# Performance work log

Measured on AMD Instinct MI355X. Metric: run time of the kernel, lower is better.

The kernel has to match this reference:

```python
import jax, jax.numpy as jnp
import numpy as np

N, E, D, H = 50000, 1600000, 256, 256
EPS = 1e-5

def prelu(x, a):
    return jnp.where(x >= 0, x, a * x)

def batch_norm(x, gamma, beta):
    # training-mode BatchNorm1d: stats over the node (batch) dim
    mu = jnp.mean(x, axis=0)
    var = jnp.var(x, axis=0)
    return (x - mu) * jax.lax.rsqrt(var + EPS) * gamma + beta

def gcn_conv(x, edge_index, W, b):
    # PyG GCNConv: h = XW, add self-loops, symmetric norm, scatter-add, + bias
    h = x @ W
    n = x.shape[0]
    row = jnp.concatenate([edge_index[0], jnp.arange(n)])
    col = jnp.concatenate([edge_index[1], jnp.arange(n)])
    w = jnp.ones(row.shape[0], dtype=x.dtype)
    deg = jax.ops.segment_sum(w, col, num_segments=n)
    dinv = jnp.where(deg > 0, jax.lax.rsqrt(deg), 0.0)
    norm = dinv[row] * w * dinv[col]  # [E+N]
    msg = h[row] * norm[:, None]      # [E+N, H] gathered messages
    out = jax.ops.segment_sum(msg, col, num_segments=n)
    return out + b

def setup_inputs() -> dict:
    key = jax.random.key(0)
    ks = jax.random.split(key, 10)
    x = jax.random.normal(ks[0], (N, D), dtype=jnp.float32)
    edge_index = jax.random.randint(ks[1], (2, E), 0, N).astype(jnp.int64)
    s1 = 1.0 / np.sqrt(D)
    s2 = 1.0 / np.sqrt(H)
    return {
        "x": x,
        "edge_index": edge_index,
        "W1": jax.random.uniform(ks[2], (D, H), jnp.float32, -s1, s1),
        "b1": jnp.zeros((H,), jnp.float32),
        "W2": jax.random.uniform(ks[3], (H, H), jnp.float32, -s2, s2),
        "b2": jnp.zeros((H,), jnp.float32),
        "prelu_a": jnp.asarray(0.25, jnp.float32),
        "bn_gamma": jnp.ones((H,), jnp.float32),
        "bn_beta": jnp.zeros((H,), jnp.float32),
        "proj_W": jax.random.uniform(ks[4], (H, H), jnp.float32, -s2, s2),
        "proj_b": jnp.zeros((H,), jnp.float32),
        "pbn_gamma": jnp.ones((H,), jnp.float32),
        "pbn_beta": jnp.zeros((H,), jnp.float32),
        "prelu2_a": jnp.asarray(0.25, jnp.float32),
    }

def reference(x, edge_index, W1, b1, W2, b2, prelu_a, bn_gamma, bn_beta,
              proj_W, proj_b, pbn_gamma, pbn_beta, prelu2_a):
    # eval-mode dropout (identity); BN uses batch stats
    z = prelu(gcn_conv(x, edge_index, W1, b1), prelu_a)
    z = prelu(gcn_conv(z, edge_index, W2, b2), prelu_a)
    z = batch_norm(z, bn_gamma, bn_beta)
    p = prelu(batch_norm(z @ proj_W + proj_b, pbn_gamma, pbn_beta), prelu2_a)
    return (z, p)
```

## Files before the change

### kernel.cpp

```cpp
#include <hip/hip_runtime.h>
#include <hip/hip_bf16.h>


#define CAP 96
#define NPB 128
#define NPART 8
#define SEGCAP 768

typedef __attribute__((ext_vector_type(8))) short short8;
typedef __attribute__((ext_vector_type(4))) float f32x4;

__device__ __forceinline__ float bf2f(unsigned short u) {
    union { unsigned int i; float f; } v; v.i = ((unsigned int)u) << 16; return v.f;
}
__device__ __forceinline__ unsigned short f2bf(float f) {
    __hip_bfloat16 h = __float2bfloat16(f);
    return *reinterpret_cast<unsigned short*>(&h);
}

__global__ __launch_bounds__(256) void k_zero(int* segcnt, int nseg, float* stats, float* dinv, int N) {
    int i = blockIdx.x * 256 + threadIdx.x;
    if (i < nseg) segcnt[i] = 0;
    if (i < 2048) stats[i] = 0.0f;
    if (i == 0) dinv[N] = 0.0f;
}

__global__ __launch_bounds__(256) void k_bin(const int* __restrict__ row, const int* __restrict__ col,
                                             unsigned* __restrict__ bins, int* __restrict__ segcnt, int E) {
    int e = blockIdx.x * 256 + threadIdx.x;
    if (e >= E) return;
    int v = col[e];
    int r = row[e];
    int seg = (v >> 7) * NPART + (blockIdx.x & (NPART - 1));
    int p = atomicAdd(&segcnt[seg], 1);
    if (p < SEGCAP) bins[(size_t)seg * SEGCAP + p] = ((unsigned)r << 7) | (unsigned)(v & (NPB - 1));
}

__global__ __launch_bounds__(256) void k_csr(const unsigned* __restrict__ bins, const int* __restrict__ segcnt,
                                             int* __restrict__ csr, int* __restrict__ fillp,
                                             float* __restrict__ dinv, int N) {
    __shared__ int cnt[NPB];
    int bkt = blockIdx.x;
    if (threadIdx.x < NPB) cnt[threadIdx.x] = 0;
    __syncthreads();
    for (int part = 0; part < NPART; ++part) {
        int seg = bkt * NPART + part;
        int m = segcnt[seg]; if (m > SEGCAP) m = SEGCAP;
        const unsigned* b = bins + (size_t)seg * SEGCAP;
        for (int i = threadIdx.x; i < m; i += 256) {
            unsigned ent = b[i];
            int loc = (int)(ent & (NPB - 1));
            int r   = (int)(ent >> 7);
            int p = atomicAdd(&cnt[loc], 1);
            if (p < CAP) csr[(size_t)(bkt * NPB + loc) * CAP + p] = r;
        }
    }
    __syncthreads();
    if (threadIdx.x < NPB) {
        int v = bkt * NPB + threadIdx.x;
        if (v < N) {
            int c = cnt[threadIdx.x];
            int real = c < CAP ? c : CAP;
            int pc = (real + 7) & ~7;
            if (pc > CAP) pc = CAP;
            int* lst = csr + (size_t)v * CAP;
            for (int p = real; p < pc; ++p) lst[p] = N;
            fillp[v] = pc;
            dinv[v] = rsqrtf(1.0f + (float)c);
        }
    }
}

__global__ __launch_bounds__(256) void k_castx(const float* __restrict__ x, unsigned short* __restrict__ xb, size_t n4) {
    size_t stride = (size_t)gridDim.x * blockDim.x;
    for (size_t i = (size_t)blockIdx.x * blockDim.x + threadIdx.x; i < n4; i += stride) {
        float4 v = ((const float4*)x)[i];
        ushort4 o; o.x = f2bf(v.x); o.y = f2bf(v.y); o.z = f2bf(v.z); o.w = f2bf(v.w);
        ((ushort4*)xb)[i] = o;
    }
}

__global__ __launch_bounds__(256) void k_wt(const float* __restrict__ W, unsigned short* __restrict__ Wt) {
    __shared__ float t[32][33];
    int bx = blockIdx.x * 32, by = blockIdx.y * 32;
    int x = threadIdx.x & 31, y = threadIdx.x >> 5;
#pragma unroll
    for (int i = 0; i < 32; i += 8)
        t[y + i][x] = W[(size_t)(by + y + i) * 256 + bx + x];
    __syncthreads();
#pragma unroll
    for (int i = 0; i < 32; i += 8)
        Wt[(size_t)(bx + y + i) * 256 + by + x] = f2bf(t[x][y + i]);
}

__global__ __launch_bounds__(256) void k_gemm_bf16(const unsigned short* __restrict__ A,
                                                   const unsigned short* __restrict__ Bt,
                                                   unsigned short* __restrict__ C, int M) {
    __shared__ unsigned short As[128 * 64];
    __shared__ unsigned short Bs[128 * 64];
    int tid  = threadIdx.x;
    int lane = tid & 63, wid = tid >> 6;
    int wr = wid >> 1, wc = wid & 1;
    int row0 = blockIdx.x * 128;
    int col0 = blockIdx.y * 128;

    f32x4 acc[4][4];
#pragma unroll
    for (int m = 0; m < 4; ++m)
#pragma unroll
        for (int n = 0; n < 4; ++n) acc[m][n] = f32x4{0.f, 0.f, 0.f, 0.f};

    int srow = lane >> 3;
    int sk   = (lane & 7) * 8;

    for (int k0 = 0; k0 < 256; k0 += 64) {
#pragma unroll
        for (int i = 0; i < 4; ++i) {
            int u = i * 4 + wid;
            int arow = row0 + u * 8 + srow;
            if (arow >= M) arow = M - 1;
            const unsigned short* ga = A  + (size_t)arow * 256 + k0 + sk;
            const unsigned short* gb = Bt + (size_t)(col0 + u * 8 + srow) * 256 + k0 + sk;
            __builtin_amdgcn_global_load_lds((const __attribute__((address_space(1))) void*)ga,
                (__attribute__((address_space(3))) void*)(As + u * 512), 16, 0, 0);
            __builtin_amdgcn_global_load_lds((const __attribute__((address_space(1))) void*)gb,
                (__attribute__((address_space(3))) void*)(Bs + u * 512), 16, 0, 0);
        }
        __syncthreads();
#pragma unroll
        for (int kk = 0; kk < 64; kk += 32) {
            short8 a[4], b[4];
#pragma unroll
            for (int m = 0; m < 4; ++m)
                a[m] = *(const short8*)(As + (wr * 64 + m * 16 + (lane & 15)) * 64 + kk + (lane >> 4) * 8);
#pragma unroll
            for (int n = 0; n < 4; ++n)
                b[n] = *(const short8*)(Bs + (wc * 64 + n * 16 + (lane & 15)) * 64 + kk + (lane >> 4) * 8);
#pragma unroll
            for (int m = 0; m < 4; ++m)
#pragma unroll
                for (int n = 0; n < 4; ++n)
                    acc[m][n] = __builtin_amdgcn_mfma_f32_16x16x32_bf16(a[m], b[n], acc[m][n], 0, 0, 0);
        }
        __syncthreads();
    }

    int crow = row0 + wr * 64;
    int ccol = col0 + wc * 64;
#pragma unroll
    for (int m = 0; m < 4; ++m)
#pragma unroll
        for (int r = 0; r < 4; ++r) {
            int rr = crow + m * 16 + (lane >> 4) * 4 + r;
            if (rr < M) {
#pragma unroll
                for (int n = 0; n < 4; ++n)
                    C[(size_t)rr * 256 + ccol + n * 16 + (lane & 15)] = f2bf(acc[m][n][r]);
            }
        }
}

__global__ __launch_bounds__(256) void k_agg_bf(const unsigned short* __restrict__ h,
                                                unsigned short* __restrict__ outb,
                                                const float* __restrict__ dinv, const int* __restrict__ csr,
                                                const int* __restrict__ fillp, const float* __restrict__ bias,
                                                const float* __restrict__ aptr, int N) {
    int wv = threadIdx.x >> 6, lane = threadIdx.x & 63;
    int v = blockIdx.x * 4 + wv;
    if (v >= N) return;
    const ushort4* h4 = (const ushort4*)h;
    float dv = dinv[v];
    ushort4 hv = h4[(size_t)v * 64 + lane];
    float s0 = dv * bf2f(hv.x), s1 = dv * bf2f(hv.y), s2 = dv * bf2f(hv.z), s3 = dv * bf2f(hv.w);
    int n = fillp[v];
    const int* lst = csr + (size_t)v * CAP;
    for (int i = 0; i < n; i += 8) {
        int u0 = lst[i],     u1 = lst[i + 1], u2 = lst[i + 2], u3 = lst[i + 3];
        int u4 = lst[i + 4], u5 = lst[i + 5], u6 = lst[i + 6], u7 = lst[i + 7];
        ushort4 a0 = h4[(size_t)u0 * 64 + lane];
        ushort4 a1 = h4[(size_t)u1 * 64 + lane];
        ushort4 a2 = h4[(size_t)u2 * 64 + lane];
        ushort4 a3 = h4[(size_t)u3 * 64 + lane];
        ushort4 a4 = h4[(size_t)u4 * 64 + lane];
        ushort4 a5 = h4[(size_t)u5 * 64 + lane];
        ushort4 a6 = h4[(size_t)u6 * 64 + lane];
        ushort4 a7 = h4[(size_t)u7 * 64 + lane];
        float d0 = dinv[u0], d1 = dinv[u1], d2 = dinv[u2], d3 = dinv[u3];
        float d4 = dinv[u4], d5 = dinv[u5], d6 = dinv[u6], d7 = dinv[u7];
        s0 += d0 * bf2f(a0.x) + d1 * bf2f(a1.x) + d2 * bf2f(a2.x) + d3 * bf2f(a3.x)
            + d4 * bf2f(a4.x) + d5 * bf2f(a5.x) + d6 * bf2f(a6.x) + d7 * bf2f(a7.x);
        s1 += d0 * bf2f(a0.y) + d1 * bf2f(a1.y) + d2 * bf2f(a2.y) + d3 * bf2f(a3.y)
            + d4 * bf2f(a4.y) + d5 * bf2f(a5.y) + d6 * bf2f(a6.y) + d7 * bf2f(a7.y);
        s2 += d0 * bf2f(a0.z) + d1 * bf2f(a1.z) + d2 * bf2f(a2.z) + d3 * bf2f(a3.z)
            + d4 * bf2f(a4.z) + d5 * bf2f(a5.z) + d6 * bf2f(a6.z) + d7 * bf2f(a7.z);
        s3 += d0 * bf2f(a0.w) + d1 * bf2f(a1.w) + d2 * bf2f(a2.w) + d3 * bf2f(a3.w)
            + d4 * bf2f(a4.w) + d5 * bf2f(a5.w) + d6 * bf2f(a6.w) + d7 * bf2f(a7.w);
    }
    float a = *aptr;
    float4 bb = *(const float4*)(bias + lane * 4);
    float o0 = dv * s0 + bb.x, o1 = dv * s1 + bb.y, o2 = dv * s2 + bb.z, o3 = dv * s3 + bb.w;
    o0 = o0 >= 0.f ? o0 : a * o0;
    o1 = o1 >= 0.f ? o1 : a * o1;
    o2 = o2 >= 0.f ? o2 : a * o2;
    o3 = o3 >= 0.f ? o3 : a * o3;
    ushort4 o; o.x = f2bf(o0); o.y = f2bf(o1); o.z = f2bf(o2); o.w = f2bf(o3);
    ((ushort4*)outb)[(size_t)v * 64 + lane] = o;
}

__global__ __launch_bounds__(256) void k_bnstats_v(const unsigned short* __restrict__ X, float* __restrict__ sums, int N) {
    int w = threadIdx.x >> 6, lane = threadIdx.x & 63;
    int c4 = lane * 4;
    float4 s = {0.f, 0.f, 0.f, 0.f}, q = {0.f, 0.f, 0.f, 0.f};
    int rstride = gridDim.x * 4;
    for (int r = blockIdx.x * 4 + w; r < N; r += rstride) {
        ushort4 x4 = ((const ushort4*)X)[(size_t)r * 64 + lane];
        float a = bf2f(x4.x), b = bf2f(x4.y), c = bf2f(x4.z), d = bf2f(x4.w);
        s.x += a; s.y += b; s.z += c; s.w += d;
        q.x += a * a; q.y += b * b; q.z += c * c; q.w += d * d;
    }
    atomicAdd(&sums[c4 + 0], s.x); atomicAdd(&sums[c4 + 1], s.y);
    atomicAdd(&sums[c4 + 2], s.z); atomicAdd(&sums[c4 + 3], s.w);
    atomicAdd(&sums[256 + c4 + 0], q.x); atomicAdd(&sums[256 + c4 + 1], q.y);
    atomicAdd(&sums[256 + c4 + 2], q.z); atomicAdd(&sums[256 + c4 + 3], q.w);
}

__global__ __launch_bounds__(256) void k_bnfinal(float* stats, const float* __restrict__ gamma,
                                                 const float* __restrict__ beta, float invN) {
    int c = threadIdx.x;
    float mu = stats[c] * invN;
    float var = stats[256 + c] * invN - mu * mu;
    float rstd = rsqrtf(var + 1e-5f);
    float sc = rstd * gamma[c];
    stats[512 + c] = sc;
    stats[768 + c] = beta[c] - mu * sc;
}

__global__ __launch_bounds__(256) void k_bnapply_z(const unsigned short* __restrict__ in,
                                                   float* __restrict__ zout, unsigned short* __restrict__ zb,
                                                   const float* __restrict__ scale, const float* __restrict__ shift,
                                                   size_t n4) {
    size_t stride = (size_t)gridDim.x * blockDim.x;
    for (size_t i = (size_t)blockIdx.x * blockDim.x + threadIdx.x; i < n4; i += stride) {
        int c4 = (int)(i & 63) * 4;
        ushort4 x4 = ((const ushort4*)in)[i];
        float4 sc = *(const float4*)(scale + c4);
        float4 sh = *(const float4*)(shift + c4);
        float4 y;
        y.x = bf2f(x4.x) * sc.x + sh.x;
        y.y = bf2f(x4.y) * sc.y + sh.y;
        y.z = bf2f(x4.z) * sc.z + sh.z;
        y.w = bf2f(x4.w) * sc.w + sh.w;
        ((float4*)zout)[i] = y;
        ushort4 o; o.x = f2bf(y.x); o.y = f2bf(y.y); o.z = f2bf(y.z); o.w = f2bf(y.w);
        ((ushort4*)zb)[i] = o;
    }
}

__global__ __launch_bounds__(256) void k_bnapply_p(const unsigned short* __restrict__ in,
                                                   float* __restrict__ pout,
                                                   const float* __restrict__ scale, const float* __restrict__ shift,
                                                   const float* __restrict__ aptr, size_t n4) {
    size_t stride = (size_t)gridDim.x * blockDim.x;
    float a = *aptr;
    for (size_t i = (size_t)blockIdx.x * blockDim.x + threadIdx.x; i < n4; i += stride) {
        int c4 = (int)(i & 63) * 4;
        ushort4 x4 = ((const ushort4*)in)[i];
        float4 sc = *(const float4*)(scale + c4);
        float4 sh = *(const float4*)(shift + c4);
        float4 y;
        y.x = bf2f(x4.x) * sc.x + sh.x;
        y.y = bf2f(x4.y) * sc.y + sh.y;
        y.z = bf2f(x4.z) * sc.z + sh.z;
        y.w = bf2f(x4.w) * sc.w + sh.w;
        y.x = y.x >= 0.f ? y.x : a * y.x;
        y.y = y.y >= 0.f ? y.y : a * y.y;
        y.z = y.z >= 0.f ? y.z : a * y.z;
        y.w = y.w >= 0.f ? y.w : a * y.w;
        ((float4*)pout)[i] = y;
    }
}

extern "C" void kernel_launch(void* const* d_in, const int* in_sizes, int n_in,
                              void* d_out, int out_size, void* d_ws, size_t ws_size,
                              hipStream_t stream) {
    const float* x     = (const float*)d_in[0];
    const int*   ei    = (const int*)d_in[1];
    const float* W1    = (const float*)d_in[2];
    const float* b1    = (const float*)d_in[3];
    const float* W2    = (const float*)d_in[4];
    const float* b2    = (const float*)d_in[5];
    const float* aptr  = (const float*)d_in[6];
    const float* gamma = (const float*)d_in[7];
    const float* beta  = (const float*)d_in[8];
    const float* projW = (const float*)d_in[9];
    const float* pgamma = (const float*)d_in[11];
    const float* pbeta  = (const float*)d_in[12];
    const float* a2ptr  = (const float*)d_in[13];

    int N = in_sizes[0] / 256;
    int E = in_sizes[1] / 2;
    const int* row = ei;
    const int* col = ei + E;

    float* out  = (float*)d_out;
    float* zout = out;
    float* pout = out + (size_t)N * 256;

    int nbkt = (N + NPB - 1) / NPB;
    int nseg = nbkt * NPART;

    unsigned short* B0 = (unsigned short*)d_ws;
    unsigned short* B1 = B0 + (size_t)N * 256;
    unsigned short* B2 = B1 + (size_t)N * 256;
    unsigned short* Wt = B2 + (size_t)N * 256;
    float* dinv  = (float*)(Wt + 3 * 65536);
    int*   fillp = (int*)(dinv + N + 1);
    int*   csr   = fillp + N;
    float* stats = (float*)(csr + (size_t)N * CAP);
    int*   segcnt= (int*)(stats + 2048);
    unsigned* bins = (unsigned*)B1;

    int nb_E = (E + 255) / 256;
    dim3 ggrid((N + 127) / 128, 2);
    dim3 wgrid(8, 8);
    int  agrid = (N + 3) / 4;
    size_t n4 = (size_t)N * 64;

    k_zero <<<(nseg + 2303) / 256, 256, 0, stream>>>(segcnt, nseg, stats, dinv, N);
    k_bin  <<<nb_E, 256, 0, stream>>>(row, col, bins, segcnt, E);
    k_csr  <<<nbkt, 256, 0, stream>>>(bins, segcnt, csr, fillp, dinv, N);
    k_castx<<<2048, 256, 0, stream>>>(x, B0, n4);
    k_wt   <<<wgrid, 256, 0, stream>>>(W1,    Wt);
    k_wt   <<<wgrid, 256, 0, stream>>>(W2,    Wt + 65536);
    k_wt   <<<wgrid, 256, 0, stream>>>(projW, Wt + 131072);

    k_gemm_bf16<<<ggrid, 256, 0, stream>>>(B0, Wt, B1, N);
    k_agg_bf   <<<agrid, 256, 0, stream>>>(B1, B2, dinv, csr, fillp, b1, aptr, N);
    k_gemm_bf16<<<ggrid, 256, 0, stream>>>(B2, Wt + 65536, B1, N);
    k_agg_bf   <<<agrid, 256, 0, stream>>>(B1, B0, dinv, csr, fillp, b2, aptr, N);
    k_bnstats_v<<<128, 256, 0, stream>>>(B0, stats, N);
    k_bnfinal  <<<1, 256, 0, stream>>>(stats, gamma, beta, 1.0f / (float)N);
    k_bnapply_z<<<2048, 256, 0, stream>>>(B0, zout, B2, stats + 512, stats + 768, n4);
    k_gemm_bf16<<<ggrid, 256, 0, stream>>>(B2, Wt + 131072, B1, N);
    k_bnstats_v<<<128, 256, 0, stream>>>(B1, stats + 1024, N);
    k_bnfinal  <<<1, 256, 0, stream>>>(stats + 1024, pgamma, pbeta, 1.0f / (float)N);
    k_bnapply_p<<<2048, 256, 0, stream>>>(B1, pout, stats + 1536, stats + 1792, a2ptr, n4);
}
```

Measured before the change: 790.8 us.

## Bin edges with per-block shared histograms instead of global per-edge atomics

Replaces the per-edge global atomic binning into 8 partitioned segments with a two-pass per-block shared-memory histogram. Each block reserves contiguous ranges per bucket with one global atomic per bucket, then scatters edges locally. The CSR build then reads one larger segment per bucket. This cuts global atomic contention, but each block reads col twice and the bins now live in a separate workspace region after segcnt.

```diff
diff --git a/kernel.cpp b/kernel.cpp
--- a/kernel.cpp
+++ b/kernel.cpp
@@ -4,8 +4,9 @@
 
 #define CAP 96
 #define NPB 128
-#define NPART 8
-#define SEGCAP 768
+#define CHUNK 4096
+#define SEGBIG 4608
+#define MAXBKT 512
 
 typedef __attribute__((ext_vector_type(8))) short short8;
 typedef __attribute__((ext_vector_type(4))) float f32x4;
@@ -18,22 +19,37 @@
     return *reinterpret_cast<unsigned short*>(&h);
 }
 
-__global__ __launch_bounds__(256) void k_zero(int* segcnt, int nseg, float* stats, float* dinv, int N) {
+__global__ __launch_bounds__(256) void k_zero(int* segcnt, int nbkt, float* stats, float* dinv, int N) {
     int i = blockIdx.x * 256 + threadIdx.x;
-    if (i < nseg) segcnt[i] = 0;
+    if (i < nbkt) segcnt[i] = 0;
     if (i < 2048) stats[i] = 0.0f;
     if (i == 0) dinv[N] = 0.0f;
 }
 
-__global__ __launch_bounds__(256) void k_bin(const int* __restrict__ row, const int* __restrict__ col,
-                                             unsigned* __restrict__ bins, int* __restrict__ segcnt, int E) {
-    int e = blockIdx.x * 256 + threadIdx.x;
-    if (e >= E) return;
-    int v = col[e];
-    int r = row[e];
-    int seg = (v >> 7) * NPART + (blockIdx.x & (NPART - 1));
-    int p = atomicAdd(&segcnt[seg], 1);
-    if (p < SEGCAP) bins[(size_t)seg * SEGCAP + p] = ((unsigned)r << 7) | (unsigned)(v & (NPB - 1));
+__global__ __launch_bounds__(256) void k_binh(const int* __restrict__ row, const int* __restrict__ col,
+                                              unsigned* __restrict__ bins, int* __restrict__ segcnt,
+                                              int E, int nbkt) {
+    __shared__ int hist[MAXBKT];
+    __shared__ int base[MAXBKT];
+    int e0 = blockIdx.x * CHUNK;
+    int eend = e0 + CHUNK; if (eend > E) eend = E;
+    for (int b = threadIdx.x; b < nbkt; b += 256) hist[b] = 0;
+    __syncthreads();
+    for (int e = e0 + threadIdx.x; e < eend; e += 256)
+        atomicAdd(&hist[col[e] >> 7], 1);
+    __syncthreads();
+    for (int b = threadIdx.x; b < nbkt; b += 256) {
+        int h = hist[b];
+        base[b] = h ? atomicAdd(&segcnt[b], h) : 0;
+        hist[b] = 0;
+    }
+    __syncthreads();
+    for (int e = e0 + threadIdx.x; e < eend; e += 256) {
+        int v = col[e], r = row[e];
+        int b = v >> 7;
+        int p = base[b] + atomicAdd(&hist[b], 1);
+        if (p < SEGBIG) bins[(size_t)b * SEGBIG + p] = ((unsigned)r << 7) | (unsigned)(v & (NPB - 1));
+    }
 }
 
 __global__ __launch_bounds__(256) void k_csr(const unsigned* __restrict__ bins, const int* __restrict__ segcnt,
@@ -43,17 +59,14 @@
     int bkt = blockIdx.x;
     if (threadIdx.x < NPB) cnt[threadIdx.x] = 0;
     __syncthreads();
-    for (int part = 0; part < NPART; ++part) {
-        int seg = bkt * NPART + part;
-        int m = segcnt[seg]; if (m > SEGCAP) m = SEGCAP;
-        const unsigned* b = bins + (size_t)seg * SEGCAP;
-        for (int i = threadIdx.x; i < m; i += 256) {
-            unsigned ent = b[i];
-            int loc = (int)(ent & (NPB - 1));
-            int r   = (int)(ent >> 7);
-            int p = atomicAdd(&cnt[loc], 1);
-            if (p < CAP) csr[(size_t)(bkt * NPB + loc) * CAP + p] = r;
-        }
+    int m = segcnt[bkt]; if (m > SEGBIG) m = SEGBIG;
+    const unsigned* b = bins + (size_t)bkt * SEGBIG;
+    for (int i = threadIdx.x; i < m; i += 256) {
+        unsigned ent = b[i];
+        int loc = (int)(ent & (NPB - 1));
+        int r   = (int)(ent >> 7);
+        int p = atomicAdd(&cnt[loc], 1);
+        if (p < CAP) csr[(size_t)(bkt * NPB + loc) * CAP + p] = r;
     }
     __syncthreads();
     if (threadIdx.x < NPB) {
@@ -307,7 +320,6 @@
     float* pout = out + (size_t)N * 256;
 
     int nbkt = (N + NPB - 1) / NPB;
-    int nseg = nbkt * NPART;
 
     unsigned short* B0 = (unsigned short*)d_ws;
     unsigned short* B1 = B0 + (size_t)N * 256;
@@ -318,16 +330,16 @@
     int*   csr   = fillp + N;
     float* stats = (float*)(csr + (size_t)N * CAP);
     int*   segcnt= (int*)(stats + 2048);
-    unsigned* bins = (unsigned*)B1;
-
-    int nb_E = (E + 255) / 256;
+    unsigned* bins = (unsigned*)(segcnt + MAXBKT);
+
+    int nb_binh = (E + CHUNK - 1) / CHUNK;
     dim3 ggrid((N + 127) / 128, 2);
     dim3 wgrid(8, 8);
     int  agrid = (N + 3) / 4;
     size_t n4 = (size_t)N * 64;
 
-    k_zero <<<(nseg + 2303) / 256, 256, 0, stream>>>(segcnt, nseg, stats, dinv, N);
-    k_bin  <<<nb_E, 256, 0, stream>>>(row, col, bins, segcnt, E);
+    k_zero <<<(2048 + 255) / 256, 256, 0, stream>>>(segcnt, nbkt, stats, dinv, N);
+    k_binh <<<nb_binh, 256, 0, stream>>>(row, col, bins, segcnt, E, nbkt);
     k_csr  <<<nbkt, 256, 0, stream>>>(bins, segcnt, csr, fillp, dinv, N);
     k_castx<<<2048, 256, 0, stream>>>(x, B0, n4);
     k_wt   <<<wgrid, 256, 0, stream>>>(W1,    Wt);
```

Result: faster. 682.4 us (-13.7%).
